# Kernel optimization log

Hardware: AMD Instinct MI355X
Metric: run time of the kernel (lower is better)

## Reference

```python
import jax, jax.numpy as jnp
import numpy as np

NU, NS, DIM, H, DEG, B = 100000, 200000, 64, 2, 8, 16384
HD = H * DIM

def _edges(key, n, deg):
    # random edges plus self-loops (DGL add_self_loop) so every dst has >=1 edge
    src = jax.random.randint(key, (n * deg,), 0, n, dtype=jnp.int32)
    dst = jax.random.randint(jax.random.fold_in(key, 1), (n * deg,), 0, n, dtype=jnp.int32)
    loop = jnp.arange(n, dtype=jnp.int32)
    return jnp.concatenate([src, loop]), jnp.concatenate([dst, loop])

def setup_inputs() -> dict:
    key = jax.random.key(0)
    ks = jax.random.split(key, 24)
    u_src, u_dst = _edges(ks[0], NU, DEG)
    s_src, s_dst = _edges(ks[1], NS, DEG)
    g = lambda k, shp, scale=0.1: jax.random.normal(k, shp, jnp.float32) * scale
    return {
        'userIdx': jax.random.randint(ks[2], (B,), 0, NU, dtype=jnp.int32),
        'servIdx': jax.random.randint(ks[3], (B,), 0, NS, dtype=jnp.int32),
        'u_src': u_src, 'u_dst': u_dst, 's_src': s_src, 's_dst': s_dst,
        'user_emb': g(ks[4], (NU, DIM), 1.0), 'serv_emb': g(ks[5], (NS, DIM), 1.0),
        'u_W': g(ks[6], (DIM, HD)), 'u_attn_l': g(ks[7], (H, DIM)), 'u_attn_r': g(ks[8], (H, DIM)),
        'u_bias': jnp.zeros((HD,), jnp.float32), 'u_ln_g': jnp.ones((HD,), jnp.float32), 'u_ln_b': jnp.zeros((HD,), jnp.float32),
        's_W': g(ks[9], (DIM, HD)), 's_attn_l': g(ks[10], (H, DIM)), 's_attn_r': g(ks[11], (H, DIM)),
        's_bias': jnp.zeros((HD,), jnp.float32), 's_ln_g': jnp.ones((HD,), jnp.float32), 's_ln_b': jnp.zeros((HD,), jnp.float32),
        'W1': g(ks[12], (2 * DIM, 128)), 'b1': jnp.zeros((128,), jnp.float32),
        'ln1_g': jnp.ones((128,), jnp.float32), 'ln1_b': jnp.zeros((128,), jnp.float32),
        'W2': g(ks[13], (128, 128)), 'b2': jnp.zeros((128,), jnp.float32),
        'ln2_g': jnp.ones((128,), jnp.float32), 'ln2_b': jnp.zeros((128,), jnp.float32),
        'W3': g(ks[14], (128, 1)), 'b3': jnp.zeros((1,), jnp.float32),
    }

def _layernorm(x, g, b, eps=1e-5):
    mu = jnp.mean(x, -1, keepdims=True)
    var = jnp.mean(jnp.square(x - mu), -1, keepdims=True)
    return (x - mu) * jax.lax.rsqrt(var + eps) * g + b

def _gat_block(feat, src, dst, W, al, ar, bias, ln_g, ln_b, n):
    # DGL GATConv (eval: dropout = identity), then LayerNorm + ELU + head-mean
    h = (feat @ W).reshape(n, H, DIM)                  # [N,H,D]
    el = jnp.sum(h * al, -1)                           # [N,H]
    er = jnp.sum(h * ar, -1)
    e = jax.nn.leaky_relu(el[src] + er[dst], 0.2)      # [E,H]
    m = jax.ops.segment_max(e, dst, num_segments=n)    # edge softmax per dst
    ex = jnp.exp(e - m[dst])
    den = jax.ops.segment_sum(ex, dst, num_segments=n)
    alpha = ex / den[dst]                              # [E,H]
    out = jax.ops.segment_sum(alpha[:, :, None] * h[src], dst, num_segments=n)
    out = out.reshape(n, HD) + bias                    # [N,H*D]
    out = jax.nn.elu(_layernorm(out, ln_g, ln_b))
    return jnp.mean(out.reshape(n, H, DIM), axis=1)    # [N,D]

def reference(userIdx, servIdx, u_src, u_dst, s_src, s_dst, user_emb, serv_emb,
              u_W, u_attn_l, u_attn_r, u_bias, u_ln_g, u_ln_b,
              s_W, s_attn_l, s_attn_r, s_bias, s_ln_g, s_ln_b,
              W1, b1, ln1_g, ln1_b, W2, b2, ln2_g, ln2_b, W3, b3):
    ug = _gat_block(user_emb, u_src, u_dst, u_W, u_attn_l, u_attn_r, u_bias, u_ln_g, u_ln_b, NU)
    sg = _gat_block(serv_emb, s_src, s_dst, s_W, s_attn_l, s_attn_r, s_bias, s_ln_g, s_ln_b, NS)
    ue = ug[userIdx] + user_emb[userIdx]               # agg == 'add'
    se = sg[servIdx] + serv_emb[servIdx]
    x = jnp.concatenate([ue, se], axis=-1)             # [B, 2*DIM]
    x = jax.nn.relu(_layernorm(x @ W1 + b1, ln1_g, ln1_b))
    x = jax.nn.relu(_layernorm(x @ W2 + b2, ln2_g, ln2_b))
    return jax.nn.sigmoid(x @ W3 + b3).reshape(-1)
```

## Files before the change

### kernel.cpp

```cpp
#include <hip/hip_runtime.h>
#include <cstdint>
#include <cstddef>

__device__ __forceinline__ float rl_f32(float v, int lane) {
    return __uint_as_float((unsigned)__builtin_amdgcn_readlane((int)__float_as_uint(v), lane));
}
__device__ __forceinline__ float wave_sum(float v) {
#pragma unroll
    for (int o = 32; o > 0; o >>= 1) v += __shfl_xor(v, o, 64);
    return v;
}
__device__ __forceinline__ float wave_max(float v) {
#pragma unroll
    for (int o = 32; o > 0; o >>= 1) v = fmaxf(v, __shfl_xor(v, o, 64));
    return v;
}

__global__ void prep_kernel(const float* __restrict__ u_W, const float* __restrict__ u_al,
                            const float* __restrict__ u_ar, float4* __restrict__ wq_u,
                            const float* __restrict__ s_W, const float* __restrict__ s_al,
                            const float* __restrict__ s_ar, float4* __restrict__ wq_s) {
    int t = threadIdx.x;
    const float *W, *al, *ar; float4* wq; int k;
    if (t < 64) { W = u_W; al = u_al; ar = u_ar; wq = wq_u; k = t; }
    else        { W = s_W; al = s_al; ar = s_ar; wq = wq_s; k = t - 64; }
    float a0 = 0.f, a1 = 0.f, a2 = 0.f, a3 = 0.f;
    for (int d = 0; d < 64; ++d) {
        float w0 = W[k * 128 + d], w1 = W[k * 128 + 64 + d];
        a0 += w0 * al[d];      a1 += w1 * al[64 + d];
        a2 += w0 * ar[d];      a3 += w1 * ar[64 + d];
    }
    wq[k] = make_float4(a0, a1, a2, a3);
}

__global__ void zero_kernel(unsigned* __restrict__ cnt_u, unsigned char* __restrict__ mark_u, int nU,
                            unsigned* __restrict__ cnt_s, unsigned char* __restrict__ mark_s, int nS) {
    int i = blockIdx.x * blockDim.x + threadIdx.x;
    int tot = nU + nS;
    if (i >= tot) return;
    if (i < nU) { cnt_u[i] = 0u; mark_u[i] = 0; }
    else        { cnt_s[i - nU] = 0u; mark_s[i - nU] = 0; }
}

__global__ void mark_kernel(const int* __restrict__ uIdx, unsigned char* __restrict__ mark_u,
                            const int* __restrict__ sIdx, unsigned char* __restrict__ mark_s, int B) {
    int t = blockIdx.x * blockDim.x + threadIdx.x;
    if (t < B)          mark_u[uIdx[t]] = 1;
    else if (t < 2 * B) mark_s[sIdx[t - B]] = 1;
}

__global__ void count_kernel(const int* __restrict__ u_dst, int EU, unsigned* __restrict__ cnt_u,
                             const unsigned char* __restrict__ mark_u,
                             const int* __restrict__ s_dst, int ES, unsigned* __restrict__ cnt_s,
                             const unsigned char* __restrict__ mark_s) {
    int e = blockIdx.x * blockDim.x + threadIdx.x;
    int tot = EU + ES;
    if (e >= tot) return;
    if (e < EU) {
        int d = u_dst[e];
        if (mark_u[d]) atomicAdd(&cnt_u[d], 1u);
    } else {
        int d = s_dst[e - EU];
        if (mark_s[d]) atomicAdd(&cnt_s[d], 1u);
    }
}

#define SCAN_TPB 256
#define SCAN_VPT 8
#define SCAN_TILE 2048

__global__ __launch_bounds__(SCAN_TPB) void scan1_kernel(
    const unsigned* __restrict__ cnt_u, unsigned* __restrict__ indptr_u, unsigned* __restrict__ sums_u, int nU, int nbU,
    const unsigned* __restrict__ cnt_s, unsigned* __restrict__ indptr_s, unsigned* __restrict__ sums_s, int nS) {
    int b = (int)blockIdx.x;
    const unsigned* cnt; unsigned* indptr; unsigned* sums; int n, tile;
    if (b < nbU) { cnt = cnt_u; indptr = indptr_u; sums = sums_u; n = nU; tile = b; }
    else         { cnt = cnt_s; indptr = indptr_s; sums = sums_s; n = nS; tile = b - nbU; }
    int base = tile * SCAN_TILE + (int)threadIdx.x * SCAN_VPT;
    unsigned v[SCAN_VPT];
#pragma unroll
    for (int j = 0; j < SCAN_VPT; ++j) { int i = base + j; v[j] = (i < n) ? cnt[i] : 0u; }
#pragma unroll
    for (int j = 1; j < SCAN_VPT; ++j) v[j] += v[j - 1];
    __shared__ unsigned sh[SCAN_TPB];
    sh[threadIdx.x] = v[SCAN_VPT - 1];
    __syncthreads();
    for (int d = 1; d < SCAN_TPB; d <<= 1) {
        unsigned t = (threadIdx.x >= (unsigned)d) ? sh[threadIdx.x - d] : 0u;
        __syncthreads();
        sh[threadIdx.x] += t;
        __syncthreads();
    }
    unsigned prefix = (threadIdx.x > 0) ? sh[threadIdx.x - 1] : 0u;
#pragma unroll
    for (int j = 0; j < SCAN_VPT; ++j) { int i = base + j; if (i < n) indptr[i + 1] = v[j] + prefix; }
    if (threadIdx.x == SCAN_TPB - 1) sums[tile] = sh[SCAN_TPB - 1];
}

__global__ void scan2_kernel(unsigned* __restrict__ sums_u, int nbU, unsigned* __restrict__ sums_s, int nbS) {
    unsigned* sums = (blockIdx.x == 0) ? sums_u : sums_s;
    int nb = (blockIdx.x == 0) ? nbU : nbS;
    __shared__ unsigned sh[256];
    int t = threadIdx.x;
    sh[t] = (t < nb) ? sums[t] : 0u;
    __syncthreads();
    if (t == 0) {
        unsigned run = 0;
        for (int i = 0; i < nb; ++i) { unsigned c = sh[i]; sh[i] = run; run += c; }
    }
    __syncthreads();
    if (t < nb) sums[t] = sh[t];
}

__global__ __launch_bounds__(SCAN_TPB) void scan3_kernel(
    const unsigned* __restrict__ cnt_u, unsigned* __restrict__ indptr_u, unsigned* __restrict__ fill_u,
    const unsigned* __restrict__ sums_u, int nU, int nbU,
    const unsigned* __restrict__ cnt_s, unsigned* __restrict__ indptr_s, unsigned* __restrict__ fill_s,
    const unsigned* __restrict__ sums_s, int nS) {
    int b = (int)blockIdx.x;
    const unsigned* cnt; unsigned* indptr; unsigned* fill; const unsigned* sums; int n, tile;
    if (b < nbU) { cnt = cnt_u; indptr = indptr_u; fill = fill_u; sums = sums_u; n = nU; tile = b; }
    else         { cnt = cnt_s; indptr = indptr_s; fill = fill_s; sums = sums_s; n = nS; tile = b - nbU; }
    unsigned off = sums[tile];
    int base = tile * SCAN_TILE + (int)threadIdx.x * SCAN_VPT;
#pragma unroll
    for (int j = 0; j < SCAN_VPT; ++j) {
        int i = base + j;
        if (i < n) {
            unsigned incl = indptr[i + 1] + off;
            indptr[i + 1] = incl;
            fill[i] = incl - cnt[i];
        }
    }
    if (b == 0 && threadIdx.x == 0) { indptr_u[0] = 0u; indptr_s[0] = 0u; }
}

__global__ void scatter_kernel(const int* __restrict__ u_src, const int* __restrict__ u_dst, int EU,
                               unsigned* __restrict__ fill_u, unsigned* __restrict__ csr_u,
                               const unsigned char* __restrict__ mark_u,
                               const int* __restrict__ s_src, const int* __restrict__ s_dst, int ES,
                               unsigned* __restrict__ fill_s, unsigned* __restrict__ csr_s,
                               const unsigned char* __restrict__ mark_s) {
    int e = blockIdx.x * blockDim.x + threadIdx.x;
    int tot = EU + ES;
    if (e >= tot) return;
    if (e < EU) {
        int d = u_dst[e];
        if (mark_u[d]) {
            unsigned pos = atomicAdd(&fill_u[d], 1u);
            csr_u[pos] = (unsigned)u_src[e];
        }
    } else {
        int ee = e - EU;
        int d = s_dst[ee];
        if (mark_s[d]) {
            unsigned pos = atomicAdd(&fill_s[d], 1u);
            csr_s[pos] = (unsigned)s_src[ee];
        }
    }
}

__global__ void eler_kernel(const float* __restrict__ user_emb, const float4* __restrict__ wq_u,
                            float4* __restrict__ elr_u, int nU,
                            const float* __restrict__ serv_emb, const float4* __restrict__ wq_s,
                            float4* __restrict__ elr_s, int nS) {
    int n = blockIdx.x * blockDim.x + threadIdx.x;
    int tot = nU + nS;
    if (n >= tot) return;
    const float* feat; const float4* wq; float4* elr; int i;
    if (n < nU) { i = n;      feat = user_emb + (size_t)i * 64; wq = wq_u; elr = elr_u; }
    else        { i = n - nU; feat = serv_emb + (size_t)i * 64; wq = wq_s; elr = elr_s; }
    float a0 = 0.f, a1 = 0.f, a2 = 0.f, a3 = 0.f;
    const float4* f4 = (const float4*)feat;
#pragma unroll
    for (int q = 0; q < 16; ++q) {
        float4 f = f4[q];
        float4 w;
        w = wq[q * 4 + 0]; a0 += f.x * w.x; a1 += f.x * w.y; a2 += f.x * w.z; a3 += f.x * w.w;
        w = wq[q * 4 + 1]; a0 += f.y * w.x; a1 += f.y * w.y; a2 += f.y * w.z; a3 += f.y * w.w;
        w = wq[q * 4 + 2]; a0 += f.z * w.x; a1 += f.z * w.y; a2 += f.z * w.z; a3 += f.z * w.w;
        w = wq[q * 4 + 3]; a0 += f.w * w.x; a1 += f.w * w.y; a2 += f.w * w.z; a3 += f.w * w.w;
    }
    elr[i] = make_float4(a0, a1, a2, a3);
}

#define AGG_RPB 8
__global__ __launch_bounds__(256) void agg_kernel(
    const int* __restrict__ uIdx, const unsigned* __restrict__ indptr_u, const unsigned* __restrict__ csr_u,
    const float* __restrict__ elr_u, const float* __restrict__ user_emb, const float* __restrict__ u_W,
    const float* __restrict__ u_bias, const float* __restrict__ u_g, const float* __restrict__ u_b,
    const int* __restrict__ sIdx, const unsigned* __restrict__ indptr_s, const unsigned* __restrict__ csr_s,
    const float* __restrict__ elr_s, const float* __restrict__ serv_emb, const float* __restrict__ s_W,
    const float* __restrict__ s_bias, const float* __restrict__ s_g, const float* __restrict__ s_b,
    float* __restrict__ xbuf, int B, int nBlocksU) {
    __shared__ float2 Wp[64 * 64];
    bool isU = (int)blockIdx.x < nBlocksU;
    const int* idx; const unsigned* indptr; const unsigned* csr; const float* elr;
    const float* emb; const float* W; const float* bias; const float* g; const float* bb;
    int bbase;
    if (isU) {
        idx = uIdx; indptr = indptr_u; csr = csr_u; elr = elr_u; emb = user_emb; W = u_W;
        bias = u_bias; g = u_g; bb = u_b; bbase = (int)blockIdx.x * AGG_RPB;
    } else {
        idx = sIdx; indptr = indptr_s; csr = csr_s; elr = elr_s; emb = serv_emb; W = s_W;
        bias = s_bias; g = s_g; bb = s_b; bbase = ((int)blockIdx.x - nBlocksU) * AGG_RPB;
    }
    for (int t = threadIdx.x; t < 4096; t += 256) {
        int k = t >> 6, l = t & 63;
        Wp[t] = make_float2(W[k * 128 + l], W[k * 128 + 64 + l]);
    }
    __syncthreads();

    int wid = threadIdx.x >> 6, lane = threadIdx.x & 63;
    int xoff = isU ? 0 : 64;
    const float2* elr2 = (const float2*)elr;

    for (int b = bbase + wid; b < bbase + AGG_RPB && b < B; b += 4) {
        int d = idx[b];
        unsigned s = indptr[d];
        int deg = (int)(indptr[d + 1] - s);
        float2 erp = elr2[(size_t)d * 2 + 1];
        float er0 = erp.x, er1 = erp.y;

        float agg0 = 0.f, agg1 = 0.f;
        if (deg <= 64) {
            unsigned mysrc = 0;
            if (lane < deg) mysrc = csr[s + lane];
            float2 elp = elr2[(size_t)mysrc * 2];
            float e0 = elp.x + er0; e0 = e0 > 0.f ? e0 : 0.2f * e0;
            float e1 = elp.y + er1; e1 = e1 > 0.f ? e1 : 0.2f * e1;
            if (lane >= deg) { e0 = -1e30f; e1 = -1e30f; }
            float m0 = wave_max(e0), m1 = wave_max(e1);
            float p0 = (lane < deg) ? expf(e0 - m0) : 0.f;
            float p1 = (lane < deg) ? expf(e1 - m1) : 0.f;
            float sum0 = wave_sum(p0), sum1 = wave_sum(p1);
            float alpha0 = p0 * (1.0f / sum0);
            float alpha1 = p1 * (1.0f / sum1);

            for (int cb = 0; cb < deg; cb += 16) {
                float f[16];
#pragma unroll
                for (int jj = 0; jj < 16; ++jj) {
                    int j2 = cb + jj;
                    if (j2 < deg) {
                        unsigned sj = (unsigned)__builtin_amdgcn_readlane((int)mysrc, j2);
                        f[jj] = emb[(size_t)sj * 64 + lane];
                    } else f[jj] = 0.f;
                }
#pragma unroll
                for (int jj = 0; jj < 16; ++jj) {
                    int j2 = cb + jj;
                    if (j2 < deg) {
                        float a0 = rl_f32(alpha0, j2);
                        float a1 = rl_f32(alpha1, j2);
                        agg0 = fmaf(a0, f[jj], agg0);
                        agg1 = fmaf(a1, f[jj], agg1);
                    }
                }
            }
        } else {
            float m0 = -1e30f, m1 = -1e30f;
            for (int j = lane; j < deg; j += 64) {
                int src = (int)csr[s + j];
                float2 elp = elr2[(size_t)src * 2];
                float e0 = elp.x + er0; e0 = e0 > 0.f ? e0 : 0.2f * e0;
                float e1 = elp.y + er1; e1 = e1 > 0.f ? e1 : 0.2f * e1;
                m0 = fmaxf(m0, e0); m1 = fmaxf(m1, e1);
            }
            m0 = wave_max(m0); m1 = wave_max(m1);
            float s0 = 0.f, s1 = 0.f;
            for (int j = lane; j < deg; j += 64) {
                int src = (int)csr[s + j];
                float2 elp = elr2[(size_t)src * 2];
                float e0 = elp.x + er0; e0 = e0 > 0.f ? e0 : 0.2f * e0;
                float e1 = elp.y + er1; e1 = e1 > 0.f ? e1 : 0.2f * e1;
                s0 += expf(e0 - m0); s1 += expf(e1 - m1);
            }
            s0 = wave_sum(s0); s1 = wave_sum(s1);
            float r0 = 1.0f / s0, r1 = 1.0f / s1;
            for (int j = 0; j < deg; ++j) {
                int src = (int)csr[s + j];
                float2 elp = elr2[(size_t)src * 2];
                float e0 = elp.x + er0; e0 = e0 > 0.f ? e0 : 0.2f * e0;
                float e1 = elp.y + er1; e1 = e1 > 0.f ? e1 : 0.2f * e1;
                float a0 = expf(e0 - m0) * r0;
                float a1 = expf(e1 - m1) * r1;
                float f = emb[(size_t)src * 64 + lane];
                agg0 = fmaf(a0, f, agg0); agg1 = fmaf(a1, f, agg1);
            }
        }

        float acc0 = 0.f, acc1 = 0.f;
#pragma unroll
        for (int k = 0; k < 64; ++k) {
            float a0 = rl_f32(agg0, k);
            float a1 = rl_f32(agg1, k);
            float2 w = Wp[k * 64 + lane];
            acc0 = fmaf(a0, w.x, acc0);
            acc1 = fmaf(a1, w.y, acc1);
        }

        float o0 = acc0 + bias[lane], o1 = acc1 + bias[64 + lane];
        float tot = wave_sum(o0 + o1);
        float mu = tot * (1.0f / 128.0f);
        float d0 = o0 - mu, d1 = o1 - mu;
        float var = wave_sum(d0 * d0 + d1 * d1) * (1.0f / 128.0f);
        float rstd = rsqrtf(var + 1e-5f);
        float l0 = d0 * rstd * g[lane] + bb[lane];
        float l1 = d1 * rstd * g[64 + lane] + bb[64 + lane];
        l0 = l0 > 0.f ? l0 : expm1f(l0);
        l1 = l1 > 0.f ? l1 : expm1f(l1);
        float v = 0.5f * (l0 + l1) + emb[(size_t)d * 64 + lane];
        xbuf[(size_t)b * 128 + xoff + lane] = v;
    }
}

#define MLP_BLOCKS 512
__global__ __launch_bounds__(256) void mlp_kernel(const float* __restrict__ xin, float* __restrict__ xout,
                                                  const float* __restrict__ W, const float* __restrict__ bvec,
                                                  const float* __restrict__ g, const float* __restrict__ bb,
                                                  int B) {
    __shared__ float2 Wp[128 * 64];
    for (int t = threadIdx.x; t < 8192; t += 256) {
        int k = t >> 6, l = t & 63;
        Wp[t] = make_float2(W[k * 128 + l], W[k * 128 + 64 + l]);
    }
    __syncthreads();
    int wid = threadIdx.x >> 6, lane = threadIdx.x & 63;
    for (int r = (int)blockIdx.x * 4 + wid; r < B; r += MLP_BLOCKS * 4) {
        float x0 = xin[(size_t)r * 128 + lane];
        float x1 = xin[(size_t)r * 128 + 64 + lane];
        float acc0 = 0.f, acc1 = 0.f;
#pragma unroll
        for (int k = 0; k < 64; ++k) {
            float xv = rl_f32(x0, k);
            float2 w = Wp[k * 64 + lane];
            acc0 = fmaf(xv, w.x, acc0); acc1 = fmaf(xv, w.y, acc1);
        }
#pragma unroll
        for (int k = 0; k < 64; ++k) {
            float xv = rl_f32(x1, k);
            float2 w = Wp[(64 + k) * 64 + lane];
            acc0 = fmaf(xv, w.x, acc0); acc1 = fmaf(xv, w.y, acc1);
        }
        float o0 = acc0 + bvec[lane], o1 = acc1 + bvec[64 + lane];
        float tot = wave_sum(o0 + o1);
        float mu = tot * (1.0f / 128.0f);
        float d0 = o0 - mu, d1 = o1 - mu;
        float var = wave_sum(d0 * d0 + d1 * d1) * (1.0f / 128.0f);
        float rstd = rsqrtf(var + 1e-5f);
        float l0 = d0 * rstd * g[lane] + bb[lane];
        float l1 = d1 * rstd * g[64 + lane] + bb[64 + lane];
        l0 = fmaxf(l0, 0.f); l1 = fmaxf(l1, 0.f);
        xout[(size_t)r * 128 + lane] = l0;
        xout[(size_t)r * 128 + 64 + lane] = l1;
    }
}

__global__ void mlp3_kernel(const float* __restrict__ y, const float* __restrict__ W3,
                            const float* __restrict__ b3, float* __restrict__ out, int B) {
    int r = blockIdx.x * blockDim.x + threadIdx.x;
    if (r >= B) return;
    const float4* yy = (const float4*)(y + (size_t)r * 128);
    const float4* ww = (const float4*)W3;
    float acc = 0.f;
#pragma unroll
    for (int q = 0; q < 32; ++q) {
        float4 f = yy[q]; float4 w = ww[q];
        acc += f.x * w.x + f.y * w.y + f.z * w.z + f.w * w.w;
    }
    acc += b3[0];
    out[r] = 1.0f / (1.0f + expf(-acc));
}

extern "C" void kernel_launch(void* const* d_in, const int* in_sizes, int n_in,
                              void* d_out, int out_size, void* d_ws, size_t ws_size,
                              hipStream_t stream) {
    const int*   userIdx  = (const int*)d_in[0];
    const int*   servIdx  = (const int*)d_in[1];
    const int*   u_src    = (const int*)d_in[2];
    const int*   u_dst    = (const int*)d_in[3];
    const int*   s_src    = (const int*)d_in[4];
    const int*   s_dst    = (const int*)d_in[5];
    const float* user_emb = (const float*)d_in[6];
    const float* serv_emb = (const float*)d_in[7];
    const float* u_W      = (const float*)d_in[8];
    const float* u_al     = (const float*)d_in[9];
    const float* u_ar     = (const float*)d_in[10];
    const float* u_bias   = (const float*)d_in[11];
    const float* u_ln_g   = (const float*)d_in[12];
    const float* u_ln_b   = (const float*)d_in[13];
    const float* s_W      = (const float*)d_in[14];
    const float* s_al     = (const float*)d_in[15];
    const float* s_ar     = (const float*)d_in[16];
    const float* s_bias   = (const float*)d_in[17];
    const float* s_ln_g   = (const float*)d_in[18];
    const float* s_ln_b   = (const float*)d_in[19];
    const float* W1       = (const float*)d_in[20];
    const float* b1       = (const float*)d_in[21];
    const float* ln1_g    = (const float*)d_in[22];
    const float* ln1_b    = (const float*)d_in[23];
    const float* W2       = (const float*)d_in[24];
    const float* b2       = (const float*)d_in[25];
    const float* ln2_g    = (const float*)d_in[26];
    const float* ln2_b    = (const float*)d_in[27];
    const float* W3       = (const float*)d_in[28];
    const float* b3       = (const float*)d_in[29];

    const int B  = in_sizes[0];
    const int EU = in_sizes[2];
    const int ES = in_sizes[4];
    const int NU = in_sizes[6] / 64;
    const int NS = in_sizes[7] / 64;

    char* w = (char*)d_ws;
    size_t off = 0;
    auto alloc = [&](size_t bytes) -> void* {
        void* p = w + off;
        off = (off + bytes + 255) & ~(size_t)255;
        return p;
    };
    float4*   wq_u     = (float4*)  alloc(64 * sizeof(float4));
    float4*   wq_s     = (float4*)  alloc(64 * sizeof(float4));
    unsigned* cnt_u    = (unsigned*)alloc((size_t)NU * 4);
    unsigned char* mark_u = (unsigned char*)alloc((size_t)NU);
    unsigned* indptr_u = (unsigned*)alloc((size_t)(NU + 1) * 4);
    unsigned* fill_u   = (unsigned*)alloc((size_t)NU * 4);
    unsigned* csr_u    = (unsigned*)alloc((size_t)EU * 4);
    unsigned* cnt_s    = (unsigned*)alloc((size_t)NS * 4);
    unsigned char* mark_s = (unsigned char*)alloc((size_t)NS);
    unsigned* indptr_s = (unsigned*)alloc((size_t)(NS + 1) * 4);
    unsigned* fill_s   = (unsigned*)alloc((size_t)NS * 4);
    unsigned* csr_s    = (unsigned*)alloc((size_t)ES * 4);
    unsigned* sums_u   = (unsigned*)alloc(256 * 4);
    unsigned* sums_s   = (unsigned*)alloc(256 * 4);
    float*    elr_u    = (float*)   alloc((size_t)NU * 4 * sizeof(float));
    float*    elr_s    = (float*)   alloc((size_t)NS * 4 * sizeof(float));
    float*    xbuf     = (float*)   alloc((size_t)B * 128 * sizeof(float));
    float*    ybuf     = (float*)   alloc((size_t)B * 128 * sizeof(float));
    (void)ws_size;

    const int nbU = (NU + SCAN_TILE - 1) / SCAN_TILE;
    const int nbS = (NS + SCAN_TILE - 1) / SCAN_TILE;
    const int totN = NU + NS;
    const int totE = EU + ES;

    prep_kernel<<<1, 128, 0, stream>>>(u_W, u_al, u_ar, wq_u, s_W, s_al, s_ar, wq_s);
    zero_kernel<<<(totN + 255) / 256, 256, 0, stream>>>(cnt_u, mark_u, NU, cnt_s, mark_s, NS);
    mark_kernel<<<(2 * B + 255) / 256, 256, 0, stream>>>(userIdx, mark_u, servIdx, mark_s, B);
    count_kernel<<<(totE + 255) / 256, 256, 0, stream>>>(u_dst, EU, cnt_u, mark_u,
                                                         s_dst, ES, cnt_s, mark_s);
    scan1_kernel<<<nbU + nbS, SCAN_TPB, 0, stream>>>(cnt_u, indptr_u, sums_u, NU, nbU,
                                                     cnt_s, indptr_s, sums_s, NS);
    scan2_kernel<<<2, 256, 0, stream>>>(sums_u, nbU, sums_s, nbS);
    scan3_kernel<<<nbU + nbS, SCAN_TPB, 0, stream>>>(cnt_u, indptr_u, fill_u, sums_u, NU, nbU,
                                                     cnt_s, indptr_s, fill_s, sums_s, NS);
    scatter_kernel<<<(totE + 255) / 256, 256, 0, stream>>>(u_src, u_dst, EU, fill_u, csr_u, mark_u,
                                                           s_src, s_dst, ES, fill_s, csr_s, mark_s);
    eler_kernel<<<(totN + 255) / 256, 256, 0, stream>>>(user_emb, wq_u, (float4*)elr_u, NU,
                                                        serv_emb, wq_s, (float4*)elr_s, NS);
    const int nBlocksU = (B + AGG_RPB - 1) / AGG_RPB;
    agg_kernel<<<2 * nBlocksU, 256, 0, stream>>>(
        userIdx, indptr_u, csr_u, elr_u, user_emb, u_W, u_bias, u_ln_g, u_ln_b,
        servIdx, indptr_s, csr_s, elr_s, serv_emb, s_W, s_bias, s_ln_g, s_ln_b,
        xbuf, B, nBlocksU);
    mlp_kernel<<<MLP_BLOCKS, 256, 0, stream>>>(xbuf, ybuf, W1, b1, ln1_g, ln1_b, B);
    mlp_kernel<<<MLP_BLOCKS, 256, 0, stream>>>(ybuf, xbuf, W2, b2, ln2_g, ln2_b, B);
    mlp3_kernel<<<(B + 255) / 256, 256, 0, stream>>>(xbuf, W3, b3, (float*)d_out, B);
}
```

Before: 447.7 us.

## Split GAT aggregation into gather and projection, fuse small kernels

Folds the attention-weight prep into eler_kernel, which now computes it into shared memory per block. The middle scan pass is merged into the final scan, with each block summing the preceding tile totals through a wave reduction. The aggregation kernel is split into a gather kernel (one wave per row, no shared weights) and a persistent projection kernel that loads W into LDS once per block. The second MLP layer and the final sigmoid layer are fused into one kernel. Together these cut launch count and per-block LDS weight loading, at the cost of an extra aggregation buffer round trip through memory and redundant weight-prep work in every eler block.

```diff
diff --git a/kernel.cpp b/kernel.cpp
--- a/kernel.cpp
+++ b/kernel.cpp
@@ -10,27 +10,15 @@
     for (int o = 32; o > 0; o >>= 1) v += __shfl_xor(v, o, 64);
     return v;
 }
+__device__ __forceinline__ unsigned wave_sum_u32(unsigned v) {
+#pragma unroll
+    for (int o = 32; o > 0; o >>= 1) v += (unsigned)__shfl_xor((int)v, o, 64);
+    return v;
+}
 __device__ __forceinline__ float wave_max(float v) {
 #pragma unroll
     for (int o = 32; o > 0; o >>= 1) v = fmaxf(v, __shfl_xor(v, o, 64));
     return v;
-}
-
-__global__ void prep_kernel(const float* __restrict__ u_W, const float* __restrict__ u_al,
-                            const float* __restrict__ u_ar, float4* __restrict__ wq_u,
-                            const float* __restrict__ s_W, const float* __restrict__ s_al,
-                            const float* __restrict__ s_ar, float4* __restrict__ wq_s) {
-    int t = threadIdx.x;
-    const float *W, *al, *ar; float4* wq; int k;
-    if (t < 64) { W = u_W; al = u_al; ar = u_ar; wq = wq_u; k = t; }
-    else        { W = s_W; al = s_al; ar = s_ar; wq = wq_s; k = t - 64; }
-    float a0 = 0.f, a1 = 0.f, a2 = 0.f, a3 = 0.f;
-    for (int d = 0; d < 64; ++d) {
-        float w0 = W[k * 128 + d], w1 = W[k * 128 + 64 + d];
-        a0 += w0 * al[d];      a1 += w1 * al[64 + d];
-        a2 += w0 * ar[d];      a3 += w1 * ar[64 + d];
-    }
-    wq[k] = make_float4(a0, a1, a2, a3);
 }
 
 __global__ void zero_kernel(unsigned* __restrict__ cnt_u, unsigned char* __restrict__ mark_u, int nU,
@@ -97,22 +85,7 @@
     if (threadIdx.x == SCAN_TPB - 1) sums[tile] = sh[SCAN_TPB - 1];
 }
 
-__global__ void scan2_kernel(unsigned* __restrict__ sums_u, int nbU, unsigned* __restrict__ sums_s, int nbS) {
-    unsigned* sums = (blockIdx.x == 0) ? sums_u : sums_s;
-    int nb = (blockIdx.x == 0) ? nbU : nbS;
-    __shared__ unsigned sh[256];
-    int t = threadIdx.x;
-    sh[t] = (t < nb) ? sums[t] : 0u;
-    __syncthreads();
-    if (t == 0) {
-        unsigned run = 0;
-        for (int i = 0; i < nb; ++i) { unsigned c = sh[i]; sh[i] = run; run += c; }
-    }
-    __syncthreads();
-    if (t < nb) sums[t] = sh[t];
-}
-
-__global__ __launch_bounds__(SCAN_TPB) void scan3_kernel(
+__global__ __launch_bounds__(SCAN_TPB) void scanf_kernel(
     const unsigned* __restrict__ cnt_u, unsigned* __restrict__ indptr_u, unsigned* __restrict__ fill_u,
     const unsigned* __restrict__ sums_u, int nU, int nbU,
     const unsigned* __restrict__ cnt_s, unsigned* __restrict__ indptr_s, unsigned* __restrict__ fill_s,
@@ -121,7 +94,10 @@
     const unsigned* cnt; unsigned* indptr; unsigned* fill; const unsigned* sums; int n, tile;
     if (b < nbU) { cnt = cnt_u; indptr = indptr_u; fill = fill_u; sums = sums_u; n = nU; tile = b; }
     else         { cnt = cnt_s; indptr = indptr_s; fill = fill_s; sums = sums_s; n = nS; tile = b - nbU; }
-    unsigned off = sums[tile];
+    int lane = threadIdx.x & 63;
+    unsigned a0 = (lane < tile) ? sums[lane] : 0u;
+    unsigned a1 = (lane + 64 < tile) ? sums[lane + 64] : 0u;
+    unsigned off = wave_sum_u32(a0 + a1);
     int base = tile * SCAN_TILE + (int)threadIdx.x * SCAN_VPT;
 #pragma unroll
     for (int j = 0; j < SCAN_VPT; ++j) {
@@ -160,51 +136,153 @@
     }
 }
 
-__global__ void eler_kernel(const float* __restrict__ user_emb, const float4* __restrict__ wq_u,
-                            float4* __restrict__ elr_u, int nU,
-                            const float* __restrict__ serv_emb, const float4* __restrict__ wq_s,
-                            float4* __restrict__ elr_s, int nS) {
-    int n = blockIdx.x * blockDim.x + threadIdx.x;
+__global__ __launch_bounds__(256) void eler_kernel(
+    const float* __restrict__ u_W, const float* __restrict__ u_al, const float* __restrict__ u_ar,
+    const float* __restrict__ s_W, const float* __restrict__ s_al, const float* __restrict__ s_ar,
+    const float* __restrict__ user_emb, float4* __restrict__ elr_u, int nU,
+    const float* __restrict__ serv_emb, float4* __restrict__ elr_s, int nS) {
+    __shared__ float4 wq[128];
+    int t = threadIdx.x;
+    if (t < 128) {
+        const float* W  = (t < 64) ? u_W : s_W;
+        const float* al = (t < 64) ? u_al : s_al;
+        const float* ar = (t < 64) ? u_ar : s_ar;
+        int k = t & 63;
+        float a0 = 0.f, a1 = 0.f, a2 = 0.f, a3 = 0.f;
+        for (int d = 0; d < 64; ++d) {
+            float w0 = W[k * 128 + d], w1 = W[k * 128 + 64 + d];
+            a0 += w0 * al[d];      a1 += w1 * al[64 + d];
+            a2 += w0 * ar[d];      a3 += w1 * ar[64 + d];
+        }
+        wq[t] = make_float4(a0, a1, a2, a3);
+    }
+    __syncthreads();
+    int n = blockIdx.x * 256 + t;
     int tot = nU + nS;
     if (n >= tot) return;
-    const float* feat; const float4* wq; float4* elr; int i;
-    if (n < nU) { i = n;      feat = user_emb + (size_t)i * 64; wq = wq_u; elr = elr_u; }
-    else        { i = n - nU; feat = serv_emb + (size_t)i * 64; wq = wq_s; elr = elr_s; }
+    const float* feat; const float4* wqp; float4* elr; int i;
+    if (n < nU) { i = n;      feat = user_emb + (size_t)i * 64; wqp = wq;      elr = elr_u; }
+    else        { i = n - nU; feat = serv_emb + (size_t)i * 64; wqp = wq + 64; elr = elr_s; }
     float a0 = 0.f, a1 = 0.f, a2 = 0.f, a3 = 0.f;
     const float4* f4 = (const float4*)feat;
 #pragma unroll
     for (int q = 0; q < 16; ++q) {
         float4 f = f4[q];
         float4 w;
-        w = wq[q * 4 + 0]; a0 += f.x * w.x; a1 += f.x * w.y; a2 += f.x * w.z; a3 += f.x * w.w;
-        w = wq[q * 4 + 1]; a0 += f.y * w.x; a1 += f.y * w.y; a2 += f.y * w.z; a3 += f.y * w.w;
-        w = wq[q * 4 + 2]; a0 += f.z * w.x; a1 += f.z * w.y; a2 += f.z * w.z; a3 += f.z * w.w;
-        w = wq[q * 4 + 3]; a0 += f.w * w.x; a1 += f.w * w.y; a2 += f.w * w.z; a3 += f.w * w.w;
+        w = wqp[q * 4 + 0]; a0 = fmaf(f.x, w.x, a0); a1 = fmaf(f.x, w.y, a1); a2 = fmaf(f.x, w.z, a2); a3 = fmaf(f.x, w.w, a3);
+        w = wqp[q * 4 + 1]; a0 = fmaf(f.y, w.x, a0); a1 = fmaf(f.y, w.y, a1); a2 = fmaf(f.y, w.z, a2); a3 = fmaf(f.y, w.w, a3);
+        w = wqp[q * 4 + 2]; a0 = fmaf(f.z, w.x, a0); a1 = fmaf(f.z, w.y, a1); a2 = fmaf(f.z, w.z, a2); a3 = fmaf(f.z, w.w, a3);
+        w = wqp[q * 4 + 3]; a0 = fmaf(f.w, w.x, a0); a1 = fmaf(f.w, w.y, a1); a2 = fmaf(f.w, w.z, a2); a3 = fmaf(f.w, w.w, a3);
     }
     elr[i] = make_float4(a0, a1, a2, a3);
 }
 
-#define AGG_RPB 8
-__global__ __launch_bounds__(256) void agg_kernel(
+__global__ __launch_bounds__(256, 8) void gather_kernel(
     const int* __restrict__ uIdx, const unsigned* __restrict__ indptr_u, const unsigned* __restrict__ csr_u,
-    const float* __restrict__ elr_u, const float* __restrict__ user_emb, const float* __restrict__ u_W,
-    const float* __restrict__ u_bias, const float* __restrict__ u_g, const float* __restrict__ u_b,
+    const float* __restrict__ elr_u, const float* __restrict__ user_emb,
     const int* __restrict__ sIdx, const unsigned* __restrict__ indptr_s, const unsigned* __restrict__ csr_s,
-    const float* __restrict__ elr_s, const float* __restrict__ serv_emb, const float* __restrict__ s_W,
-    const float* __restrict__ s_bias, const float* __restrict__ s_g, const float* __restrict__ s_b,
-    float* __restrict__ xbuf, int B, int nBlocksU) {
+    const float* __restrict__ elr_s, const float* __restrict__ serv_emb,
+    float* __restrict__ aggbuf, int B, int nBlocksU) {
+    bool isU = (int)blockIdx.x < nBlocksU;
+    const int* idx; const unsigned* indptr; const unsigned* csr; const float* elr; const float* emb;
+    int bb4 = isU ? (int)blockIdx.x : (int)blockIdx.x - nBlocksU;
+    if (isU) { idx = uIdx; indptr = indptr_u; csr = csr_u; elr = elr_u; emb = user_emb; }
+    else     { idx = sIdx; indptr = indptr_s; csr = csr_s; elr = elr_s; emb = serv_emb; }
+    int wid = threadIdx.x >> 6, lane = threadIdx.x & 63;
+    int b = bb4 * 4 + wid;
+    if (b >= B) return;
+    int row = isU ? b : B + b;
+    const float2* elr2 = (const float2*)elr;
+
+    int d = idx[b];
+    unsigned s = indptr[d];
+    int deg = (int)(indptr[d + 1] - s);
+    float2 erp = elr2[(size_t)d * 2 + 1];
+    float er0 = erp.x, er1 = erp.y;
+
+    float agg0 = 0.f, agg1 = 0.f;
+    if (deg <= 64) {
+        unsigned mysrc = 0;
+        if (lane < deg) mysrc = csr[s + lane];
+        float2 elp = elr2[(size_t)mysrc * 2];
+        float e0 = elp.x + er0; e0 = e0 > 0.f ? e0 : 0.2f * e0;
+        float e1 = elp.y + er1; e1 = e1 > 0.f ? e1 : 0.2f * e1;
+        if (lane >= deg) { e0 = -1e30f; e1 = -1e30f; }
+        float m0 = wave_max(e0), m1 = wave_max(e1);
+        float p0 = (lane < deg) ? expf(e0 - m0) : 0.f;
+        float p1 = (lane < deg) ? expf(e1 - m1) : 0.f;
+        float sum0 = wave_sum(p0), sum1 = wave_sum(p1);
+        float alpha0 = p0 * (1.0f / sum0);
+        float alpha1 = p1 * (1.0f / sum1);
+
+        for (int cb = 0; cb < deg; cb += 16) {
+            float f[16];
+#pragma unroll
+            for (int jj = 0; jj < 16; ++jj) {
+                int j2 = cb + jj;
+                if (j2 < deg) {
+                    unsigned sj = (unsigned)__builtin_amdgcn_readlane((int)mysrc, j2);
+                    f[jj] = emb[(size_t)sj * 64 + lane];
+                } else f[jj] = 0.f;
+            }
+#pragma unroll
+            for (int jj = 0; jj < 16; ++jj) {
+                int j2 = cb + jj;
+                if (j2 < deg) {
+                    agg0 = fmaf(rl_f32(alpha0, j2), f[jj], agg0);
+                    agg1 = fmaf(rl_f32(alpha1, j2), f[jj], agg1);
+                }
+            }
+        }
+    } else {
+        float m0 = -1e30f, m1 = -1e30f;
+        for (int j = lane; j < deg; j += 64) {
+            int src = (int)csr[s + j];
+            float2 elp = elr2[(size_t)src * 2];
+            float e0 = elp.x + er0; e0 = e0 > 0.f ? e0 : 0.2f * e0;
+            float e1 = elp.y + er1; e1 = e1 > 0.f ? e1 : 0.2f * e1;
+            m0 = fmaxf(m0, e0); m1 = fmaxf(m1, e1);
+        }
+        m0 = wave_max(m0); m1 = wave_max(m1);
+        float s0 = 0.f, s1 = 0.f;
+        for (int j = lane; j < deg; j += 64) {
+            int src = (int)csr[s + j];
+            float2 elp = elr2[(size_t)src * 2];
+            float e0 = elp.x + er0; e0 = e0 > 0.f ? e0 : 0.2f * e0;
+            float e1 = elp.y + er1; e1 = e1 > 0.f ? e1 : 0.2f * e1;
+            s0 += expf(e0 - m0); s1 += expf(e1 - m1);
+        }
+        s0 = wave_sum(s0); s1 = wave_sum(s1);
+        float r0 = 1.0f / s0, r1 = 1.0f / s1;
+        for (int j = 0; j < deg; ++j) {
+            int src = (int)csr[s + j];
+            float2 elp = elr2[(size_t)src * 2];
+            float e0 = elp.x + er0; e0 = e0 > 0.f ? e0 : 0.2f * e0;
+            float e1 = elp.y + er1; e1 = e1 > 0.f ? e1 : 0.2f * e1;
+            float a0 = expf(e0 - m0) * r0;
+            float a1 = expf(e1 - m1) * r1;
+            float f = emb[(size_t)src * 64 + lane];
+            agg0 = fmaf(a0, f, agg0); agg1 = fmaf(a1, f, agg1);
+        }
+    }
+
+    aggbuf[(size_t)row * 128 + lane] = agg0;
+    aggbuf[(size_t)row * 128 + 64 + lane] = agg1;
+}
+
+#define PROJ_BLOCKS 256
+__global__ __launch_bounds__(256) void proj_kernel(
+    const int* __restrict__ uIdx, const float* __restrict__ u_W, const float* __restrict__ u_bias,
+    const float* __restrict__ u_g, const float* __restrict__ u_b, const float* __restrict__ user_emb,
+    const int* __restrict__ sIdx, const float* __restrict__ s_W, const float* __restrict__ s_bias,
+    const float* __restrict__ s_g, const float* __restrict__ s_b, const float* __restrict__ serv_emb,
+    const float* __restrict__ aggbuf, float* __restrict__ xbuf, int B) {
     __shared__ float2 Wp[64 * 64];
-    bool isU = (int)blockIdx.x < nBlocksU;
-    const int* idx; const unsigned* indptr; const unsigned* csr; const float* elr;
-    const float* emb; const float* W; const float* bias; const float* g; const float* bb;
+    bool isU = (int)blockIdx.x < PROJ_BLOCKS;
+    const int* idx; const float* W; const float* bias; const float* g; const float* bb; const float* emb;
     int bbase;
-    if (isU) {
-        idx = uIdx; indptr = indptr_u; csr = csr_u; elr = elr_u; emb = user_emb; W = u_W;
-        bias = u_bias; g = u_g; bb = u_b; bbase = (int)blockIdx.x * AGG_RPB;
-    } else {
-        idx = sIdx; indptr = indptr_s; csr = csr_s; elr = elr_s; emb = serv_emb; W = s_W;
-        bias = s_bias; g = s_g; bb = s_b; bbase = ((int)blockIdx.x - nBlocksU) * AGG_RPB;
-    }
+    if (isU) { idx = uIdx; W = u_W; bias = u_bias; g = u_g; bb = u_b; emb = user_emb; bbase = (int)blockIdx.x; }
+    else     { idx = sIdx; W = s_W; bias = s_bias; g = s_g; bb = s_b; emb = serv_emb; bbase = (int)blockIdx.x - PROJ_BLOCKS; }
     for (int t = threadIdx.x; t < 4096; t += 256) {
         int k = t >> 6, l = t & 63;
         Wp[t] = make_float2(W[k * 128 + l], W[k * 128 + 64 + l]);
@@ -213,82 +291,17 @@
 
     int wid = threadIdx.x >> 6, lane = threadIdx.x & 63;
     int xoff = isU ? 0 : 64;
-    const float2* elr2 = (const float2*)elr;
-
-    for (int b = bbase + wid; b < bbase + AGG_RPB && b < B; b += 4) {
+    int rowoff = isU ? 0 : B;
+    float biasa = bias[lane], biasb = bias[64 + lane];
+    float ga = g[lane], gb2 = g[64 + lane];
+    float ba = bb[lane], bb2 = bb[64 + lane];
+
+    for (int b = bbase * 4 + wid; b < B; b += PROJ_BLOCKS * 4) {
         int d = idx[b];
-        unsigned s = indptr[d];
-        int deg = (int)(indptr[d + 1] - s);
-        float2 erp = elr2[(size_t)d * 2 + 1];
-        float er0 = erp.x, er1 = erp.y;
-
-        float agg0 = 0.f, agg1 = 0.f;
-        if (deg <= 64) {
-            unsigned mysrc = 0;
-            if (lane < deg) mysrc = csr[s + lane];
-            float2 elp = elr2[(size_t)mysrc * 2];
-            float e0 = elp.x + er0; e0 = e0 > 0.f ? e0 : 0.2f * e0;
-            float e1 = elp.y + er1; e1 = e1 > 0.f ? e1 : 0.2f * e1;
-            if (lane >= deg) { e0 = -1e30f; e1 = -1e30f; }
-            float m0 = wave_max(e0), m1 = wave_max(e1);
-            float p0 = (lane < deg) ? expf(e0 - m0) : 0.f;
-            float p1 = (lane < deg) ? expf(e1 - m1) : 0.f;
-            float sum0 = wave_sum(p0), sum1 = wave_sum(p1);
-            float alpha0 = p0 * (1.0f / sum0);
-            float alpha1 = p1 * (1.0f / sum1);
-
-            for (int cb = 0; cb < deg; cb += 16) {
-                float f[16];
-#pragma unroll
-                for (int jj = 0; jj < 16; ++jj) {
-                    int j2 = cb + jj;
-                    if (j2 < deg) {
-                        unsigned sj = (unsigned)__builtin_amdgcn_readlane((int)mysrc, j2);
-                        f[jj] = emb[(size_t)sj * 64 + lane];
-                    } else f[jj] = 0.f;
-                }
-#pragma unroll
-                for (int jj = 0; jj < 16; ++jj) {
-                    int j2 = cb + jj;
-                    if (j2 < deg) {
-                        float a0 = rl_f32(alpha0, j2);
-                        float a1 = rl_f32(alpha1, j2);
-                        agg0 = fmaf(a0, f[jj], agg0);
-                        agg1 = fmaf(a1, f[jj], agg1);
-                    }
-                }
-            }
-        } else {
-            float m0 = -1e30f, m1 = -1e30f;
-            for (int j = lane; j < deg; j += 64) {
-                int src = (int)csr[s + j];
-                float2 elp = elr2[(size_t)src * 2];
-                float e0 = elp.x + er0; e0 = e0 > 0.f ? e0 : 0.2f * e0;
-                float e1 = elp.y + er1; e1 = e1 > 0.f ? e1 : 0.2f * e1;
-                m0 = fmaxf(m0, e0); m1 = fmaxf(m1, e1);
-            }
-            m0 = wave_max(m0); m1 = wave_max(m1);
-            float s0 = 0.f, s1 = 0.f;
-            for (int j = lane; j < deg; j += 64) {
-                int src = (int)csr[s + j];
-                float2 elp = elr2[(size_t)src * 2];
-                float e0 = elp.x + er0; e0 = e0 > 0.f ? e0 : 0.2f * e0;
-                float e1 = elp.y + er1; e1 = e1 > 0.f ? e1 : 0.2f * e1;
-                s0 += expf(e0 - m0); s1 += expf(e1 - m1);
-            }
-            s0 = wave_sum(s0); s1 = wave_sum(s1);
-            float r0 = 1.0f / s0, r1 = 1.0f / s1;
-            for (int j = 0; j < deg; ++j) {
-                int src = (int)csr[s + j];
-                float2 elp = elr2[(size_t)src * 2];
-                float e0 = elp.x + er0; e0 = e0 > 0.f ? e0 : 0.2f * e0;
-                float e1 = elp.y + er1; e1 = e1 > 0.f ? e1 : 0.2f * e1;
-                float a0 = expf(e0 - m0) * r0;
-                float a1 = expf(e1 - m1) * r1;
-                float f = emb[(size_t)src * 64 + lane];
-                agg0 = fmaf(a0, f, agg0); agg1 = fmaf(a1, f, agg1);
-            }
-        }
+        float embv = emb[(size_t)d * 64 + lane];
+        int row = rowoff + b;
+        float agg0 = aggbuf[(size_t)row * 128 + lane];
+        float agg1 = aggbuf[(size_t)row * 128 + 64 + lane];
 
         float acc0 = 0.f, acc1 = 0.f;
 #pragma unroll
@@ -300,17 +313,17 @@
             acc1 = fmaf(a1, w.y, acc1);
         }
 
-        float o0 = acc0 + bias[lane], o1 = acc1 + bias[64 + lane];
+        float o0 = acc0 + biasa, o1 = acc1 + biasb;
         float tot = wave_sum(o0 + o1);
         float mu = tot * (1.0f / 128.0f);
         float d0 = o0 - mu, d1 = o1 - mu;
         float var = wave_sum(d0 * d0 + d1 * d1) * (1.0f / 128.0f);
         float rstd = rsqrtf(var + 1e-5f);
-        float l0 = d0 * rstd * g[lane] + bb[lane];
-        float l1 = d1 * rstd * g[64 + lane] + bb[64 + lane];
+        float l0 = d0 * rstd * ga + ba;
+        float l1 = d1 * rstd * gb2 + bb2;
         l0 = l0 > 0.f ? l0 : expm1f(l0);
         l1 = l1 > 0.f ? l1 : expm1f(l1);
-        float v = 0.5f * (l0 + l1) + emb[(size_t)d * 64 + lane];
+        float v = 0.5f * (l0 + l1) + embv;
         xbuf[(size_t)b * 128 + xoff + lane] = v;
     }
 }
@@ -357,20 +370,48 @@
     }
 }
 
-__global__ void mlp3_kernel(const float* __restrict__ y, const float* __restrict__ W3,
-                            const float* __restrict__ b3, float* __restrict__ out, int B) {
-    int r = blockIdx.x * blockDim.x + threadIdx.x;
-    if (r >= B) return;
-    const float4* yy = (const float4*)(y + (size_t)r * 128);
-    const float4* ww = (const float4*)W3;
-    float acc = 0.f;
-#pragma unroll
-    for (int q = 0; q < 32; ++q) {
-        float4 f = yy[q]; float4 w = ww[q];
-        acc += f.x * w.x + f.y * w.y + f.z * w.z + f.w * w.w;
-    }
-    acc += b3[0];
-    out[r] = 1.0f / (1.0f + expf(-acc));
+__global__ __launch_bounds__(256) void mlpfin_kernel(const float* __restrict__ xin, float* __restrict__ out,
+                                                     const float* __restrict__ W, const float* __restrict__ bvec,
+                                                     const float* __restrict__ g, const float* __restrict__ bb,
+                                                     const float* __restrict__ W3, const float* __restrict__ b3,
+                                                     int B) {
+    __shared__ float2 Wp[128 * 64];
+    for (int t = threadIdx.x; t < 8192; t += 256) {
+        int k = t >> 6, l = t & 63;
+        Wp[t] = make_float2(W[k * 128 + l], W[k * 128 + 64 + l]);
+    }
+    __syncthreads();
+    int wid = threadIdx.x >> 6, lane = threadIdx.x & 63;
+    float w3a = W3[lane], w3b = W3[64 + lane];
+    float b3v = b3[0];
+    for (int r = (int)blockIdx.x * 4 + wid; r < B; r += MLP_BLOCKS * 4) {
+        float x0 = xin[(size_t)r * 128 + lane];
+        float x1 = xin[(size_t)r * 128 + 64 + lane];
+        float acc0 = 0.f, acc1 = 0.f;
+#pragma unroll
+        for (int k = 0; k < 64; ++k) {
+            float xv = rl_f32(x0, k);
+            float2 w = Wp[k * 64 + lane];
+            acc0 = fmaf(xv, w.x, acc0); acc1 = fmaf(xv, w.y, acc1);
+        }
+#pragma unroll
+        for (int k = 0; k < 64; ++k) {
+            float xv = rl_f32(x1, k);
+            float2 w = Wp[(64 + k) * 64 + lane];
+            acc0 = fmaf(xv, w.x, acc0); acc1 = fmaf(xv, w.y, acc1);
+        }
+        float o0 = acc0 + bvec[lane], o1 = acc1 + bvec[64 + lane];
+        float tot = wave_sum(o0 + o1);
+        float mu = tot * (1.0f / 128.0f);
+        float d0 = o0 - mu, d1 = o1 - mu;
+        float var = wave_sum(d0 * d0 + d1 * d1) * (1.0f / 128.0f);
+        float rstd = rsqrtf(var + 1e-5f);
+        float l0 = d0 * rstd * g[lane] + bb[lane];
+        float l1 = d1 * rstd * g[64 + lane] + bb[64 + lane];
+        l0 = fmaxf(l0, 0.f); l1 = fmaxf(l1, 0.f);
+        float acc = wave_sum(fmaf(l0, w3a, l1 * w3b)) + b3v;
+        if (lane == 0) out[r] = 1.0f / (1.0f + expf(-acc));
+    }
 }
 
 extern "C" void kernel_launch(void* const* d_in, const int* in_sizes, int n_in,
@@ -420,8 +461,6 @@
         off = (off + bytes + 255) & ~(size_t)255;
         return p;
     };
-    float4*   wq_u     = (float4*)  alloc(64 * sizeof(float4));
-    float4*   wq_s     = (float4*)  alloc(64 * sizeof(float4));
     unsigned* cnt_u    = (unsigned*)alloc((size_t)NU * 4);
     unsigned char* mark_u = (unsigned char*)alloc((size_t)NU);
     unsigned* indptr_u = (unsigned*)alloc((size_t)(NU + 1) * 4);
@@ -436,8 +475,9 @@
     unsigned* sums_s   = (unsigned*)alloc(256 * 4);
     float*    elr_u    = (float*)   alloc((size_t)NU * 4 * sizeof(float));
     float*    elr_s    = (float*)   alloc((size_t)NS * 4 * sizeof(float));
+    float*    aggbuf   = (float*)   alloc((size_t)2 * B * 128 * sizeof(float));
     float*    xbuf     = (float*)   alloc((size_t)B * 128 * sizeof(float));
-    float*    ybuf     = (float*)   alloc((size_t)B * 128 * sizeof(float));
+    float*    ybuf     = aggbuf;
     (void)ws_size;
 
     const int nbU = (NU + SCAN_TILE - 1) / SCAN_TILE;
@@ -445,26 +485,28 @@
     const int totN = NU + NS;
     const int totE = EU + ES;
 
-    prep_kernel<<<1, 128, 0, stream>>>(u_W, u_al, u_ar, wq_u, s_W, s_al, s_ar, wq_s);
     zero_kernel<<<(totN + 255) / 256, 256, 0, stream>>>(cnt_u, mark_u, NU, cnt_s, mark_s, NS);
     mark_kernel<<<(2 * B + 255) / 256, 256, 0, stream>>>(userIdx, mark_u, servIdx, mark_s, B);
     count_kernel<<<(totE + 255) / 256, 256, 0, stream>>>(u_dst, EU, cnt_u, mark_u,
                                                          s_dst, ES, cnt_s, mark_s);
     scan1_kernel<<<nbU + nbS, SCAN_TPB, 0, stream>>>(cnt_u, indptr_u, sums_u, NU, nbU,
                                                      cnt_s, indptr_s, sums_s, NS);
-    scan2_kernel<<<2, 256, 0, stream>>>(sums_u, nbU, sums_s, nbS);
-    scan3_kernel<<<nbU + nbS, SCAN_TPB, 0, stream>>>(cnt_u, indptr_u, fill_u, sums_u, NU, nbU,
+    scanf_kernel<<<nbU + nbS, SCAN_TPB, 0, stream>>>(cnt_u, indptr_u, fill_u, sums_u, NU, nbU,
                                                      cnt_s, indptr_s, fill_s, sums_s, NS);
     scatter_kernel<<<(totE + 255) / 256, 256, 0, stream>>>(u_src, u_dst, EU, fill_u, csr_u, mark_u,
                                                            s_src, s_dst, ES, fill_s, csr_s, mark_s);
-    eler_kernel<<<(totN + 255) / 256, 256, 0, stream>>>(user_emb, wq_u, (float4*)elr_u, NU,
-                                                        serv_emb, wq_s, (float4*)elr_s, NS);
-    const int nBlocksU = (B + AGG_RPB - 1) / AGG_RPB;
-    agg_kernel<<<2 * nBlocksU, 256, 0, stream>>>(
-        userIdx, indptr_u, csr_u, elr_u, user_emb, u_W, u_bias, u_ln_g, u_ln_b,
-        servIdx, indptr_s, csr_s, elr_s, serv_emb, s_W, s_bias, s_ln_g, s_ln_b,
-        xbuf, B, nBlocksU);
+    eler_kernel<<<(totN + 255) / 256, 256, 0, stream>>>(u_W, u_al, u_ar, s_W, s_al, s_ar,
+                                                        user_emb, (float4*)elr_u, NU,
+                                                        serv_emb, (float4*)elr_s, NS);
+    const int nBlocksU = (B + 3) / 4;
+    gather_kernel<<<2 * nBlocksU, 256, 0, stream>>>(
+        userIdx, indptr_u, csr_u, elr_u, user_emb,
+        servIdx, indptr_s, csr_s, elr_s, serv_emb,
+        aggbuf, B, nBlocksU);
+    proj_kernel<<<2 * PROJ_BLOCKS, 256, 0, stream>>>(
+        userIdx, u_W, u_bias, u_ln_g, u_ln_b, user_emb,
+        servIdx, s_W, s_bias, s_ln_g, s_ln_b, serv_emb,
+        aggbuf, xbuf, B);
     mlp_kernel<<<MLP_BLOCKS, 256, 0, stream>>>(xbuf, ybuf, W1, b1, ln1_g, ln1_b, B);
-    mlp_kernel<<<MLP_BLOCKS, 256, 0, stream>>>(ybuf, xbuf, W2, b2, ln2_g, ln2_b, B);
-    mlp3_kernel<<<(B + 255) / 256, 256, 0, stream>>>(xbuf, W3, b3, (float*)d_out, B);
-}
+    mlpfin_kernel<<<MLP_BLOCKS, 256, 0, stream>>>(ybuf, (float*)d_out, W2, b2, ln2_g, ln2_b, W3, b3, B);
+}
```

Result: faster. 392.2 us (-12.4%).
